# Optimization experiments

Measured on AMD Instinct MI355X. Metric: run time of the kernel, lower is better.

The kernel has to match this reference:

```python
import jax, jax.numpy as jnp
import numpy as np

HIDDEN = 1024
FFN = 2048
N_EXPERTS = 8
TOP_K = 2
BSZ, Q_LEN = 1, 2048


def setup_inputs() -> dict:
    key = jax.random.key(0)
    ks = jax.random.split(key, 8)
    T = BSZ * Q_LEN
    x = jax.random.normal(ks[0], (BSZ, Q_LEN, HIDDEN), dtype=jnp.float32)
    weights = jax.random.uniform(ks[1], (T, N_EXPERTS), dtype=jnp.float32)
    top_weights = jax.random.uniform(ks[2], (T, TOP_K), dtype=jnp.float32)
    top_experts = jax.random.randint(ks[3], (T, TOP_K), 0, N_EXPERTS, dtype=jnp.int64)
    s = 0.02
    w_up = jax.random.normal(ks[4], (N_EXPERTS, HIDDEN, FFN), dtype=jnp.float32) * s
    w_gate = jax.random.normal(ks[5], (N_EXPERTS, HIDDEN, FFN), dtype=jnp.float32) * s
    w_down = jax.random.normal(ks[6], (N_EXPERTS, FFN, HIDDEN), dtype=jnp.float32) * s
    return {"x": x, "weights": weights, "top_weights": top_weights,
            "top_experts": top_experts, "w_up": w_up, "w_gate": w_gate, "w_down": w_down}


def reference(x, weights, top_weights, top_experts, w_up, w_gate, w_down):
    # x: [B, S, H]; top_experts/top_weights: [T, K]; weights unused (parity with torch forward)
    B, S, H = x.shape
    E = w_up.shape[0]
    xf = x.reshape(-1, H)  # [T, H]
    # per-token combine weight for each expert: w_tok[t, e] = sum_k top_weights[t,k] * (top_experts[t,k]==e)
    onehot = jax.nn.one_hot(top_experts, E, dtype=x.dtype)  # [T, K, E]
    w_tok = jnp.einsum('tke,tk->te', onehot, top_weights)   # [T, E]

    def body(acc, ws):
        wu, wg, wd, we = ws  # [H,F], [H,F], [F,H], [T]
        h = jax.nn.silu(xf @ wu) * (xf @ wg)  # SwiGLU: act(up) * gate
        return acc + (h @ wd) * we[:, None], None

    out, _ = jax.lax.scan(body, jnp.zeros_like(xf), (w_up, w_gate, w_down, w_tok.T))
    return out.reshape(B, S, H)
```

## Files before the change

kernel.cpp:

```cpp
#include <hip/hip_runtime.h>
#include <hip/hip_bf16.h>
#include <stdint.h>

#define T_TOK 2048
#define HID   1024
#define FFN_  2048
#define NEXP  8
#define NPAIR 4096
#define MAXTILE 40
#define EXPELEM ((size_t)HID * FFN_)
#define NSLICE 16

typedef __bf16 bf16;
typedef __bf16 bf16x8 __attribute__((ext_vector_type(8)));
typedef __bf16 bf16x4 __attribute__((ext_vector_type(4)));
typedef float  f32x4  __attribute__((ext_vector_type(4)));
typedef float  f32x4v __attribute__((ext_vector_type(4)));
typedef unsigned int u32;

#define OFF_EXP   0
#define OFF_NT    64
#define OFF_TTE   128
#define OFF_TTM   512
#define OFF_TOK   1024
#define OFF_WGT   (OFF_TOK + 16384)
#define OFF_XG    65536
#define OFF_H1    (OFF_XG + (size_t)NPAIR*HID*2)
#define OFF_WT    (OFF_H1 + (size_t)NPAIR*FFN_*2)

__device__ __forceinline__ void gld16(const void* g, void* l) {
    __builtin_amdgcn_global_load_lds(
        (const __attribute__((address_space(1))) u32*)g,
        (__attribute__((address_space(3))) u32*)l, 16, 0, 0);
}

__global__ void __launch_bounds__(1024)
route_kernel(const uint32_t* __restrict__ te_raw,
             const float* __restrict__ top_w,
             int* __restrict__ expert_off,
             int* __restrict__ ntile_g,
             int* __restrict__ tte, int* __restrict__ ttm,
             int* __restrict__ tok, float* __restrict__ wgt)
{
    __shared__ int cnt[NSLICE][NEXP];
    __shared__ int off[NSLICE][NEXP];
    __shared__ int ebase[NEXP + 1];
    __shared__ int is64_s;
    int tid = threadIdx.x;
    int wv = tid >> 6, lane = tid & 63;

    if (wv == 0) {
        int bad = (te_raw[2 * lane + 1] != 0u);
        unsigned long long m = __ballot(bad);
        if (lane == 0) is64_s = (m == 0ull);
    }
    __syncthreads();
    int is64 = is64_s;

    int c[NEXP] = {0,0,0,0,0,0,0,0};
    int eids[4];
    #pragma unroll
    for (int it = 0; it < 4; ++it) {
        int p = wv * 256 + it * 64 + lane;
        int eid = is64 ? (int)te_raw[2*p] : (int)te_raw[p];
        eids[it] = eid;
        #pragma unroll
        for (int e = 0; e < NEXP; ++e) {
            unsigned long long m = __ballot(eid == e);
            c[e] += __popcll(m);
        }
    }
    if (lane == 0)
        #pragma unroll
        for (int e = 0; e < NEXP; ++e) cnt[wv][e] = c[e];
    __syncthreads();

    if (tid < NEXP) {
        int run = 0;
        for (int s = 0; s < NSLICE; ++s) { off[s][tid] = run; run += cnt[s][tid]; }
        ebase[tid] = run;
    }
    __syncthreads();
    if (tid == 0) {
        int s = 0;
        for (int e = 0; e < NEXP; ++e) { int t = ebase[e]; ebase[e] = s; expert_off[e] = s; s += t; }
        ebase[NEXP] = s; expert_off[NEXP] = s;
        int nt = 0;
        for (int e = 0; e < NEXP; ++e)
            for (int m = ebase[e]; m < ebase[e + 1]; m += 128) { tte[nt] = e; ttm[nt] = m; ++nt; }
        *ntile_g = nt;
    }
    __syncthreads();

    int roff[NEXP];
    #pragma unroll
    for (int e = 0; e < NEXP; ++e) roff[e] = ebase[e] + off[wv][e];
    #pragma unroll
    for (int it = 0; it < 4; ++it) {
        int p = wv * 256 + it * 64 + lane;
        int eid = eids[it];
        int dest = -1;
        #pragma unroll
        for (int e = 0; e < NEXP; ++e) {
            unsigned long long m = __ballot(eid == e);
            if (eid == e) dest = roff[e] + __popcll(m & ((1ull << lane) - 1ull));
            roff[e] += __popcll(m);
        }
        tok[dest] = p >> 1;
        wgt[dest] = top_w[p];
    }
}

__global__ void gather_kernel(const float* __restrict__ x,
                              const int* __restrict__ tok,
                              bf16* __restrict__ Xg)
{
    int p = blockIdx.x;
    int t = tok[p];
    const float4* src = (const float4*)(x + (size_t)t * HID);
    float4 v = src[threadIdx.x];
    bf16x4 o;
    o[0] = (bf16)v.x; o[1] = (bf16)v.y; o[2] = (bf16)v.z; o[3] = (bf16)v.w;
    *(bf16x4*)(Xg + (size_t)p * HID + threadIdx.x * 4) = o;
}

__global__ void __launch_bounds__(256)
transpose_v5(const float* __restrict__ in1, bf16* __restrict__ out1,
             const float* __restrict__ in2, bf16* __restrict__ out2,
             int nz1, int R, int C)
{
    __shared__ u32 tile32[4][64 * 32];
    int z = blockIdx.z;
    const float* in = (z < nz1) ? in1 : in2;
    bf16* o         = (z < nz1) ? out1 : out2;
    int e = (z < nz1) ? z : z - nz1;
    in += (size_t)e * R * C;
    o  += (size_t)e * R * C;
    int kt = blockIdx.x, nq = blockIdx.y;
    int k0 = kt * 64, c0 = nq * 256;
    int tid = threadIdx.x;
    int rbase = tid >> 6;
    int c4 = tid & 63;
    int grp = c4 >> 4, cq = c4 & 15;
    int fp0 = cq * 2;
    const float* base = in + (size_t)(k0 + rbase) * C + c0 + c4 * 4;
    f32x4v rb[16];
    #pragma unroll
    for (int it = 0; it < 16; ++it)
        rb[it] = __builtin_nontemporal_load((const f32x4v*)(base + (size_t)it * 4 * C));
    #pragma unroll
    for (int it = 0; it < 16; ++it) {
        int r = rbase + it * 4;
        union { bf16 h[2]; u32 w; } a, b;
        a.h[0] = (bf16)rb[it][0]; a.h[1] = (bf16)rb[it][1];
        b.h[0] = (bf16)rb[it][2]; b.h[1] = (bf16)rb[it][3];
        tile32[grp][r * 32 + (fp0       ^ (r & 31))] = a.w;
        tile32[grp][r * 32 + ((fp0 + 1) ^ (r & 31))] = b.w;
    }
    __syncthreads();
    int RT = R >> 6;
    #pragma unroll
    for (int it2 = 0; it2 < 8; ++it2) {
        int gg = it2 * 256 + tid;
        int group = gg >> 9, g = gg & 511;
        int f = g >> 3;
        int k8 = ((g & 7) ^ (f & 7)) * 8;
        union { bf16 h[8]; } pk;
        #pragma unroll
        for (int j = 0; j < 8; ++j) {
            u32 u = tile32[group][(k8 + j) * 32 + ((f >> 1) ^ ((k8 + j) & 31))];
            pk.h[j] = (f & 1) ? ((bf16*)&u)[1] : ((bf16*)&u)[0];
        }
        bf16* tbase = o + ((size_t)(nq * 4 + group) * RT + kt) * 4096;
        *(bf16x8*)(tbase + (size_t)g * 8) = *(bf16x8*)&pk;
    }
}

#define NGEMM (MAXTILE * (FFN_ / 64))
__global__ void __launch_bounds__(256)
fused_ug(const bf16* __restrict__ Xg,
         const bf16* __restrict__ wuT, const bf16* __restrict__ wgT,
         const int* __restrict__ expert_off, const int* __restrict__ ntile_g,
         const int* __restrict__ tte, const int* __restrict__ ttm,
         bf16* __restrict__ H1,
         const float* __restrict__ Wd, bf16* __restrict__ wdT)
{
    __shared__ char ldsbuf[32768];
    int bid = blockIdx.x;
    int tid = threadIdx.x;

    if (bid >= NGEMM) {
        u32 (*tile32)[64 * 32] = (u32 (*)[64 * 32])ldsbuf;
        int tb = bid - NGEMM;
        int e = tb >> 7;
        int rem = tb & 127;
        int nq = rem >> 5, kt = rem & 31;
        const float* in = Wd + (size_t)e * EXPELEM;
        bf16* o = wdT + (size_t)e * EXPELEM;
        int k0 = kt * 64, c0 = nq * 256;
        int rbase = tid >> 6;
        int c4 = tid & 63;
        int grp = c4 >> 4, cq = c4 & 15;
        int fp0 = cq * 2;
        const float* base = in + (size_t)(k0 + rbase) * HID + c0 + c4 * 4;
        f32x4v rb[16];
        #pragma unroll
        for (int it = 0; it < 16; ++it)
            rb[it] = __builtin_nontemporal_load((const f32x4v*)(base + (size_t)it * 4 * HID));
        #pragma unroll
        for (int it = 0; it < 16; ++it) {
            int r = rbase + it * 4;
            union { bf16 h[2]; u32 w; } a, b;
            a.h[0] = (bf16)rb[it][0]; a.h[1] = (bf16)rb[it][1];
            b.h[0] = (bf16)rb[it][2]; b.h[1] = (bf16)rb[it][3];
            tile32[grp][r * 32 + (fp0       ^ (r & 31))] = a.w;
            tile32[grp][r * 32 + ((fp0 + 1) ^ (r & 31))] = b.w;
        }
        __syncthreads();
        const int RT = FFN_ >> 6;
        #pragma unroll
        for (int it2 = 0; it2 < 8; ++it2) {
            int gg = it2 * 256 + tid;
            int group = gg >> 9, g = gg & 511;
            int f = g >> 3;
            int k8 = ((g & 7) ^ (f & 7)) * 8;
            union { bf16 h[8]; } pk;
            #pragma unroll
            for (int j = 0; j < 8; ++j) {
                u32 u = tile32[group][(k8 + j) * 32 + ((f >> 1) ^ ((k8 + j) & 31))];
                pk.h[j] = (f & 1) ? ((bf16*)&u)[1] : ((bf16*)&u)[0];
            }
            bf16* tbase = o + ((size_t)(nq * 4 + group) * RT + kt) * 4096;
            *(bf16x8*)(tbase + (size_t)g * 8) = *(bf16x8*)&pk;
        }
        return;
    }

    int ty = bid >> 5, bn = bid & 31;
    if (ty >= *ntile_g) return;
    int e = tte[ty];
    int m0 = ttm[ty];
    int p1 = expert_off[e + 1];
    int n0 = bn * 64;
    bf16* As  = (bf16*)ldsbuf;
    bf16* Bus = (bf16*)(ldsbuf + 16384);
    bf16* Bgs = (bf16*)(ldsbuf + 24576);
    int lane = tid & 63, wv = tid >> 6;
    int wm = wv >> 1, wn = wv & 1;
    int l16 = lane & 15, lhi = lane >> 4;
    f32x4 accU[4][2] = {};
    f32x4 accG[4][2] = {};

    const bf16* aptr[4]; u32 alds[4];
    #pragma unroll
    for (int c = 0; c < 4; ++c) {
        int g = c * 256 + tid;
        int r = g >> 3, pos = g & 7;
        int gr = m0 + r; if (gr >= p1) gr = p1 - 1;
        int gsrc = pos ^ (r & 7);
        aptr[c] = Xg + (size_t)gr * HID + gsrc * 8;
        alds[c] = g * 16;
    }
    size_t tb0 = (size_t)e * EXPELEM + (size_t)(n0 >> 6) * (HID >> 6) * 4096;
    const bf16* buptr[2]; const bf16* bgptr[2]; u32 blds[2];
    #pragma unroll
    for (int c = 0; c < 2; ++c) {
        int g = c * 256 + tid;
        buptr[c] = wuT + tb0 + (size_t)g * 8;
        bgptr[c] = wgT + tb0 + (size_t)g * 8;
        blds[c] = g * 16;
    }
    u32 aro[2][4], bro[2][2];
    #pragma unroll
    for (int ks = 0; ks < 2; ++ks) {
        #pragma unroll
        for (int fm = 0; fm < 4; ++fm) {
            int r = wm * 64 + fm * 16 + l16;
            aro[ks][fm] = r * 128 + ((u32)((ks * 4 + lhi) ^ (r & 7))) * 16;
        }
        #pragma unroll
        for (int fn = 0; fn < 2; ++fn) {
            int fr = wn * 32 + fn * 16 + l16;
            bro[ks][fn] = fr * 128 + ((u32)((ks * 4 + lhi) ^ (fr & 7))) * 16;
        }
    }

    for (int t = 0; t < HID / 64; ++t) {
        #pragma unroll
        for (int c = 0; c < 4; ++c) { gld16(aptr[c], (char*)As + alds[c]); aptr[c] += 64; }
        #pragma unroll
        for (int c = 0; c < 2; ++c) {
            gld16(buptr[c], (char*)Bus + blds[c]); buptr[c] += 4096;
            gld16(bgptr[c], (char*)Bgs + blds[c]); bgptr[c] += 4096;
        }
        __syncthreads();
        #pragma unroll
        for (int ks = 0; ks < 2; ++ks) {
            bf16x8 af[4];
            #pragma unroll
            for (int fm = 0; fm < 4; ++fm)
                af[fm] = *(const bf16x8*)((char*)As + aro[ks][fm]);
            #pragma unroll
            for (int fn = 0; fn < 2; ++fn) {
                bf16x8 bu = *(const bf16x8*)((char*)Bus + bro[ks][fn]);
                bf16x8 bg = *(const bf16x8*)((char*)Bgs + bro[ks][fn]);
                #pragma unroll
                for (int fm = 0; fm < 4; ++fm) {
                    accU[fm][fn] = __builtin_amdgcn_mfma_f32_16x16x32_bf16(af[fm], bu, accU[fm][fn], 0, 0, 0);
                    accG[fm][fn] = __builtin_amdgcn_mfma_f32_16x16x32_bf16(af[fm], bg, accG[fm][fn], 0, 0, 0);
                }
            }
        }
        __syncthreads();
    }
    #pragma unroll
    for (int fm = 0; fm < 4; ++fm)
    #pragma unroll
    for (int fn = 0; fn < 2; ++fn)
    #pragma unroll
    for (int rg = 0; rg < 4; ++rg) {
        int r = m0 + wm * 64 + fm * 16 + lhi * 4 + rg;
        if (r < p1) {
            float u = accU[fm][fn][rg], g = accG[fm][fn][rg];
            float h = (u / (1.f + __expf(-u))) * g;
            int fc = n0 + wn * 32 + fn * 16 + l16;
            H1[(size_t)r * FFN_ + fc] = (bf16)h;
        }
    }
}

__global__ void __launch_bounds__(256)
moe_down(const bf16* __restrict__ H1, const bf16* __restrict__ wdT,
         const int* __restrict__ expert_off, const int* __restrict__ ntile_g,
         const int* __restrict__ tte, const int* __restrict__ ttm,
         const int* __restrict__ tok, const float* __restrict__ wgt,
         float* __restrict__ out)
{
    int ty = blockIdx.y;
    if (ty >= *ntile_g) return;
    int e = tte[ty];
    int m0 = ttm[ty];
    int p1 = expert_off[e + 1];
    int n0 = blockIdx.x * 64;
    __shared__ bf16 As[128 * 64];
    __shared__ bf16 Bs [64 * 64];
    __shared__ float wgt_s[128];
    __shared__ int   tok_s[128];
    int tid = threadIdx.x, lane = tid & 63, wv = tid >> 6;
    int wm = wv >> 1, wn = wv & 1;
    int l16 = lane & 15, lhi = lane >> 4;
    if (tid < 128) {
        int r = m0 + tid;
        if (r < p1) { wgt_s[tid] = wgt[r]; tok_s[tid] = tok[r]; }
        else        { wgt_s[tid] = 0.f;    tok_s[tid] = 0; }
    }
    f32x4 acc[4][2] = {};

    const bf16* aptr[4]; u32 alds[4];
    #pragma unroll
    for (int c = 0; c < 4; ++c) {
        int g = c * 256 + tid;
        int r = g >> 3, pos = g & 7;
        int gr = m0 + r; if (gr >= p1) gr = p1 - 1;
        int gsrc = pos ^ (r & 7);
        aptr[c] = H1 + (size_t)gr * FFN_ + gsrc * 8;
        alds[c] = g * 16;
    }
    size_t tb0 = (size_t)e * EXPELEM + (size_t)(n0 >> 6) * (FFN_ >> 6) * 4096;
    const bf16* bptr[2]; u32 blds[2];
    #pragma unroll
    for (int c = 0; c < 2; ++c) {
        int g = c * 256 + tid;
        bptr[c] = wdT + tb0 + (size_t)g * 8;
        blds[c] = g * 16;
    }
    u32 aro[2][4], bro[2][2];
    #pragma unroll
    for (int ks = 0; ks < 2; ++ks) {
        #pragma unroll
        for (int fm = 0; fm < 4; ++fm) {
            int r = wm * 64 + fm * 16 + l16;
            aro[ks][fm] = r * 128 + ((u32)((ks * 4 + lhi) ^ (r & 7))) * 16;
        }
        #pragma unroll
        for (int fn = 0; fn < 2; ++fn) {
            int fr = wn * 32 + fn * 16 + l16;
            bro[ks][fn] = fr * 128 + ((u32)((ks * 4 + lhi) ^ (fr & 7))) * 16;
        }
    }

    for (int t = 0; t < FFN_ / 64; ++t) {
        #pragma unroll
        for (int c = 0; c < 4; ++c) { gld16(aptr[c], (char*)As + alds[c]); aptr[c] += 64; }
        #pragma unroll
        for (int c = 0; c < 2; ++c) { gld16(bptr[c], (char*)Bs + blds[c]); bptr[c] += 4096; }
        __syncthreads();
        #pragma unroll
        for (int ks = 0; ks < 2; ++ks) {
            bf16x8 af[4];
            #pragma unroll
            for (int fm = 0; fm < 4; ++fm)
                af[fm] = *(const bf16x8*)((char*)As + aro[ks][fm]);
            #pragma unroll
            for (int fn = 0; fn < 2; ++fn) {
                bf16x8 bd = *(const bf16x8*)((char*)Bs + bro[ks][fn]);
                #pragma unroll
                for (int fm = 0; fm < 4; ++fm)
                    acc[fm][fn] = __builtin_amdgcn_mfma_f32_16x16x32_bf16(af[fm], bd, acc[fm][fn], 0, 0, 0);
            }
        }
        __syncthreads();
    }
    #pragma unroll
    for (int fm = 0; fm < 4; ++fm)
    #pragma unroll
    for (int fn = 0; fn < 2; ++fn)
    #pragma unroll
    for (int rg = 0; rg < 4; ++rg) {
        int rl = wm * 64 + fm * 16 + lhi * 4 + rg;
        if (m0 + rl < p1) {
            float v = acc[fm][fn][rg] * wgt_s[rl];
            atomicAdd(out + (size_t)tok_s[rl] * HID + n0 + wn * 32 + fn * 16 + l16, v);
        }
    }
}

extern "C" void kernel_launch(void* const* d_in, const int* in_sizes, int n_in,
                              void* d_out, int out_size, void* d_ws, size_t ws_size,
                              hipStream_t stream)
{
    const float*    x      = (const float*)d_in[0];
    const float*    top_w  = (const float*)d_in[2];
    const uint32_t* te     = (const uint32_t*)d_in[3];
    const float*    w_up   = (const float*)d_in[4];
    const float*    w_gate = (const float*)d_in[5];
    const float*    w_down = (const float*)d_in[6];
    float* out = (float*)d_out;
    char*  ws  = (char*)d_ws;

    int*   expert_off = (int*)(ws + OFF_EXP);
    int*   ntile_g    = (int*)(ws + OFF_NT);
    int*   tte        = (int*)(ws + OFF_TTE);
    int*   ttm        = (int*)(ws + OFF_TTM);
    int*   tok        = (int*)(ws + OFF_TOK);
    float* wgt        = (float*)(ws + OFF_WGT);
    bf16*  Xg         = (bf16*)(ws + OFF_XG);
    bf16*  H1         = (bf16*)(ws + OFF_H1);
    bf16*  WT         = (bf16*)(ws + OFF_WT);
    bf16*  wuT = WT;
    bf16*  wgT = WT + 8 * EXPELEM;
    bf16*  wdT = WT + 16 * EXPELEM;

    hipMemsetAsync(out, 0, (size_t)out_size * sizeof(float), stream);
    hipLaunchKernelGGL(route_kernel, dim3(1), dim3(1024), 0, stream,
                       te, top_w, expert_off, ntile_g, tte, ttm, tok, wgt);
    hipLaunchKernelGGL(gather_kernel, dim3(NPAIR), dim3(256), 0, stream,
                       x, tok, Xg);

    hipLaunchKernelGGL(transpose_v5, dim3(HID / 64, FFN_ / 256, 16), dim3(256), 0, stream,
                       w_up, wuT, w_gate, wgT, 8, HID, FFN_);

    hipLaunchKernelGGL(fused_ug, dim3(NGEMM + 1024), dim3(256), 0, stream,
                       Xg, wuT, wgT, expert_off, ntile_g, tte, ttm, H1,
                       w_down, wdT);

    hipLaunchKernelGGL(moe_down, dim3(HID / 64, MAXTILE), dim3(256), 0, stream,
                       H1, wdT, expert_off, ntile_g, tte, ttm, tok, wgt, out);
}
```

Measured before the change: 154.2 us.

## Split up/gate GEMM into two expert halves overlapping weight transposes

The standalone transpose now converts only the first four experts' up/gate weights. The fused up/gate kernel is launched twice. The first launch computes experts 0-3 while its extra blocks transpose up/gate for experts 4-7. The second launch computes experts 4-7 while transposing the down weights. This hides more of the fp32-to-bf16 weight conversion behind GEMM work, at the cost of an extra launch and many early-exit blocks in each launch.

Result: no change. 154.4 us (+0.1%).

```diff
diff --git a/kernel.cpp b/kernel.cpp
--- a/kernel.cpp
+++ b/kernel.cpp
@@ -10,6 +10,7 @@
 #define MAXTILE 40
 #define EXPELEM ((size_t)HID * FFN_)
 #define NSLICE 16
+#define NGEMM (MAXTILE * (FFN_ / 64))
 
 typedef __bf16 bf16;
 typedef __bf16 bf16x8 __attribute__((ext_vector_type(8)));
@@ -176,14 +177,15 @@
     }
 }
 
-#define NGEMM (MAXTILE * (FFN_ / 64))
 __global__ void __launch_bounds__(256)
 fused_ug(const bf16* __restrict__ Xg,
          const bf16* __restrict__ wuT, const bf16* __restrict__ wgT,
          const int* __restrict__ expert_off, const int* __restrict__ ntile_g,
          const int* __restrict__ tte, const int* __restrict__ ttm,
-         bf16* __restrict__ H1,
-         const float* __restrict__ Wd, bf16* __restrict__ wdT)
+         int eb, int gcnt, bf16* __restrict__ H1,
+         const float* __restrict__ tin1, bf16* __restrict__ tout1,
+         const float* __restrict__ tin2, bf16* __restrict__ tout2,
+         int tnz1, int tR, int tC)
 {
     __shared__ char ldsbuf[32768];
     int bid = blockIdx.x;
@@ -192,21 +194,25 @@
     if (bid >= NGEMM) {
         u32 (*tile32)[64 * 32] = (u32 (*)[64 * 32])ldsbuf;
         int tb = bid - NGEMM;
-        int e = tb >> 7;
-        int rem = tb & 127;
-        int nq = rem >> 5, kt = rem & 31;
-        const float* in = Wd + (size_t)e * EXPELEM;
-        bf16* o = wdT + (size_t)e * EXPELEM;
+        int nkt = tR >> 6;
+        int perslice = nkt * (tC >> 8);
+        int z = tb / perslice, rem = tb - z * perslice;
+        int kt = rem % nkt, nq = rem / nkt;
+        const float* in; bf16* o; int e2;
+        if (z < tnz1) { in = tin1; o = tout1; e2 = z; }
+        else          { in = tin2; o = tout2; e2 = z - tnz1; }
+        in += (size_t)e2 * tR * tC;
+        o  += (size_t)e2 * tR * tC;
         int k0 = kt * 64, c0 = nq * 256;
         int rbase = tid >> 6;
         int c4 = tid & 63;
         int grp = c4 >> 4, cq = c4 & 15;
         int fp0 = cq * 2;
-        const float* base = in + (size_t)(k0 + rbase) * HID + c0 + c4 * 4;
+        const float* base = in + (size_t)(k0 + rbase) * tC + c0 + c4 * 4;
         f32x4v rb[16];
         #pragma unroll
         for (int it = 0; it < 16; ++it)
-            rb[it] = __builtin_nontemporal_load((const f32x4v*)(base + (size_t)it * 4 * HID));
+            rb[it] = __builtin_nontemporal_load((const f32x4v*)(base + (size_t)it * 4 * tC));
         #pragma unroll
         for (int it = 0; it < 16; ++it) {
             int r = rbase + it * 4;
@@ -217,7 +223,6 @@
             tile32[grp][r * 32 + ((fp0 + 1) ^ (r & 31))] = b.w;
         }
         __syncthreads();
-        const int RT = FFN_ >> 6;
         #pragma unroll
         for (int it2 = 0; it2 < 8; ++it2) {
             int gg = it2 * 256 + tid;
@@ -230,7 +235,7 @@
                 u32 u = tile32[group][(k8 + j) * 32 + ((f >> 1) ^ ((k8 + j) & 31))];
                 pk.h[j] = (f & 1) ? ((bf16*)&u)[1] : ((bf16*)&u)[0];
             }
-            bf16* tbase = o + ((size_t)(nq * 4 + group) * RT + kt) * 4096;
+            bf16* tbase = o + ((size_t)(nq * 4 + group) * nkt + kt) * 4096;
             *(bf16x8*)(tbase + (size_t)g * 8) = *(bf16x8*)&pk;
         }
         return;
@@ -239,6 +244,7 @@
     int ty = bid >> 5, bn = bid & 31;
     if (ty >= *ntile_g) return;
     int e = tte[ty];
+    if (e < eb || e >= eb + gcnt) return;
     int m0 = ttm[ty];
     int p1 = expert_off[e + 1];
     int n0 = bn * 64;
@@ -457,12 +463,17 @@
     hipLaunchKernelGGL(gather_kernel, dim3(NPAIR), dim3(256), 0, stream,
                        x, tok, Xg);
 
-    hipLaunchKernelGGL(transpose_v5, dim3(HID / 64, FFN_ / 256, 16), dim3(256), 0, stream,
-                       w_up, wuT, w_gate, wgT, 8, HID, FFN_);
+    hipLaunchKernelGGL(transpose_v5, dim3(HID / 64, FFN_ / 256, 8), dim3(256), 0, stream,
+                       w_up, wuT, w_gate, wgT, 4, HID, FFN_);
 
     hipLaunchKernelGGL(fused_ug, dim3(NGEMM + 1024), dim3(256), 0, stream,
-                       Xg, wuT, wgT, expert_off, ntile_g, tte, ttm, H1,
-                       w_down, wdT);
+                       Xg, wuT, wgT, expert_off, ntile_g, tte, ttm, 0, 4, H1,
+                       w_up + 4 * EXPELEM, wuT + 4 * EXPELEM,
+                       w_gate + 4 * EXPELEM, wgT + 4 * EXPELEM, 4, HID, FFN_);
+
+    hipLaunchKernelGGL(fused_ug, dim3(NGEMM + 1024), dim3(256), 0, stream,
+                       Xg, wuT, wgT, expert_off, ntile_g, tte, ttm, 4, 4, H1,
+                       w_down, wdT, w_down, wdT, 8, FFN_, HID);
 
     hipLaunchKernelGGL(moe_down, dim3(HID / 64, MAXTILE), dim3(256), 0, stream,
                        H1, wdT, expert_off, ntile_g, tte, ttm, tok, wgt, out);
```
